# Kernel tuning notes

Hardware: AMD Instinct MI355X
Metric: run time of the kernel (lower is better)

## Reference

```python
import jax, jax.numpy as jnp
import numpy as np

B, L, D, H, Dh = 4, 2048, 1024, 16, 64
DECAY_LR, A_LR, V_LR, G_LR = 64, 64, 32, 128
EPS_GN = 0.00064


def _lora(x, A, Bm, b, act):
    h = x @ A.T
    if act is not None:
        h = act(h)
    y = h @ Bm.T
    return y if b is None else y + b


def setup_inputs() -> dict:
    key = jax.random.key(0)
    ks = jax.random.split(key, 32)
    n = lambda k, shape, s=0.02: (jax.random.normal(k, shape, jnp.float32) * s)
    return {
        "x": n(ks[0], (B, L, D), 1.0),
        "v_first": n(ks[1], (B, L, H, Dh), 1.0),
        "x_r": n(ks[2], (1, 1, D)), "x_w": n(ks[3], (1, 1, D)),
        "x_k": n(ks[4], (1, 1, D)), "x_v": n(ks[5], (1, 1, D)),
        "x_a": n(ks[6], (1, 1, D)), "x_g": n(ks[7], (1, 1, D)),
        "k_k": n(ks[8], (H, Dh), 0.5), "k_a": n(ks[9], (H, Dh), 0.5),
        "r_k": n(ks[10], (H, Dh), 0.5),
        "Wr": n(ks[11], (D, D)), "Wk": n(ks[12], (D, D)),
        "Wv": n(ks[13], (D, D)), "Wo": n(ks[14], (D, D)),
        "gn_w": 1.0 + n(ks[15], (H, Dh)), "gn_b": n(ks[16], (H, Dh)),
        "w_A": n(ks[17], (DECAY_LR, D)), "w_B": n(ks[18], (D, DECAY_LR)), "w_b": n(ks[19], (D,)),
        "v_A": n(ks[20], (V_LR, D)), "v_B": n(ks[21], (D, V_LR)), "v_b": n(ks[22], (D,)),
        "a_A": n(ks[23], (A_LR, D)), "a_B": n(ks[24], (D, A_LR)), "a_b": n(ks[25], (D,)),
        "g_A": n(ks[26], (G_LR, D)), "g_B": n(ks[27], (D, G_LR)),
    }


def reference(x, v_first, x_r, x_w, x_k, x_v, x_a, x_g, k_k, k_a, r_k,
              Wr, Wk, Wv, Wo, gn_w, gn_b,
              w_A, w_B, w_b, v_A, v_B, v_b, a_A, a_B, a_b, g_A, g_B):
    Bx, Lx, Dx = x.shape
    # token shift (no cache -> zero-padded shift)
    x_prev = jnp.concatenate([jnp.zeros_like(x[:, :1]), x[:, :-1]], axis=1)
    xx = x_prev - x
    xr = x + xx * x_r
    xw = x + xx * x_w
    xk = x + xx * x_k
    xv = x + xx * x_v
    xa = x + xx * x_a
    xg = x + xx * x_g

    r = (xr @ Wr.T).reshape(Bx, Lx, H, Dh)
    k = (xk @ Wk.T).reshape(Bx, Lx, H, Dh)
    v = (xv @ Wv.T).reshape(Bx, Lx, H, Dh)
    iclr = jax.nn.sigmoid(_lora(xa, a_A, a_B, a_b, None)).reshape(Bx, Lx, H, Dh)
    gate = _lora(xg, g_A, g_B, None, jax.nn.sigmoid)  # (B,L,D)

    # layer_idx > 0: residual value mixing with v_first
    vv = jax.nn.sigmoid(_lora(xv, v_A, v_B, v_b, None)).reshape(Bx, Lx, H, Dh)
    v = v + (v_first - v) * vv

    w = jnp.exp(-0.606531 * jax.nn.sigmoid(
        _lora(xw, w_A, w_B, w_b, jnp.tanh)).reshape(Bx, Lx, H, Dh))

    kkn = k * k_k
    kk = kkn / jnp.maximum(jnp.linalg.norm(kkn, axis=-1, keepdims=True), 1e-7)
    k = k * (1.0 + (iclr - 1.0) * k_a)
    a = -kk
    b = kk * iclr

    # WKV7 generalized delta-rule scan over time
    def step(state, inp):
        rt, wt, kt, vt, at, bt = inp  # each (B,H,Dh)
        sa = jnp.einsum('bhij,bhj->bhi', state, at)
        state = (state * wt[:, :, None, :]
                 + vt[..., :, None] * kt[..., None, :]
                 + sa[..., :, None] * bt[..., None, :])
        y = jnp.einsum('bhij,bhj->bhi', state, rt)
        return state, y

    tr = lambda z: jnp.swapaxes(z, 0, 1)  # (B,L,H,Dh) -> (L,B,H,Dh)
    state0 = jnp.zeros((Bx, H, Dh, Dh), x.dtype)
    _, ys = jax.lax.scan(step, state0, (tr(r), tr(w), tr(k), tr(v), tr(a), tr(b)))
    out = jnp.swapaxes(ys, 0, 1)  # (B,L,H,Dh)

    # per-head layernorm (group norm), eps = 0.00064
    mean = out.mean(axis=-1, keepdims=True)
    var = out.var(axis=-1, keepdims=True)
    out = gn_w * (out - mean) / jnp.sqrt(var + EPS_GN) + gn_b

    out = out + jnp.sum(r * k * r_k, axis=-1, keepdims=True) * v
    out = out.reshape(Bx, Lx, Dx)
    return (out * gate) @ Wo.T
```

## Files before the change

kernel.cpp:

```cpp
#include <hip/hip_runtime.h>
#include <cmath>


#define DEV __device__ __forceinline__

typedef unsigned short u16;
typedef unsigned int u32;
typedef __bf16 bf16x8 __attribute__((ext_vector_type(8)));
typedef float f32x4 __attribute__((ext_vector_type(4)));

constexpr int Bx = 4, Lx = 2048, Dx = 1024, Hx = 16, Dh = 64;
constexpr int NTOK = Bx * Lx;
constexpr float EPS_GN = 0.00064f;
constexpr int STEP_U16 = 384;
constexpr int TB = 16;
constexpr int NB = Lx / TB;
constexpr int BATCH_U16 = TB * STEP_U16;

DEV float bf2f(u16 u) { union { u32 i; float f; } c; c.i = ((u32)u) << 16; return c.f; }
DEV u16 f2bf(float f) {
    union { float f; u32 i; } c; c.f = f;
    u32 r = c.i + 0x7FFFu + ((c.i >> 16) & 1u);
    return (u16)(r >> 16);
}
DEV void unpack2(u32 u, float& a, float& b) {
    union { u32 i; float f; } c0, c1;
    c0.i = u << 16; c1.i = u & 0xFFFF0000u;
    a = c0.f; b = c1.f;
}

template <int CTRL>
DEV float dpp_add(float v) {
    int p = __builtin_amdgcn_update_dpp(0, __float_as_int(v), CTRL, 0xF, 0xF, true);
    return v + __int_as_float(p);
}

DEV float xor32_add(float x) {
    float a = x, b = x;
    asm volatile("s_nop 1\n\tv_permlane32_swap_b32 %0, %1" : "+v"(a), "+v"(b));
    return a + b;
}

DEV float red32(float x) {
    x = dpp_add<0xB1>(x);
    x = dpp_add<0x4E>(x);
    x = dpp_add<0x141>(x);
    x = dpp_add<0x140>(x);
    return xor32_add(x);
}

__global__ __launch_bounds__(256) void conv_kernel(
    const float* s0, const float* s1, const float* s2, const float* s3,
    const float* s4, const float* s5, const float* s6, const float* s7,
    const float* s8, const float* s9, const float* s10, const float* s11,
    u16* d0, u16* d1, u16* d2, u16* d3, u16* d4, u16* d5, u16* d6, u16* d7,
    u16* d8, u16* d9, u16* d10, u16* d11)
{
    const float* srcs[12] = {s0,s1,s2,s3,s4,s5,s6,s7,s8,s9,s10,s11};
    u16* dsts[12] = {d0,d1,d2,d3,d4,d5,d6,d7,d8,d9,d10,d11};
    const int ns[12] = {65536,65536,32768,32768,65536,65536,131072,131072,
                        1048576,1048576,1048576,1048576};
    int t = blockIdx.y;
    int i = (blockIdx.x * 256 + threadIdx.x) * 4;
    if (i >= ns[t]) return;
    float4 v = *(const float4*)(srcs[t] + i);
    ushort4 o;
    o.x = f2bf(v.x); o.y = f2bf(v.y); o.z = f2bf(v.z); o.w = f2bf(v.w);
    *(ushort4*)(dsts[t] + i) = o;
}

__global__ __launch_bounds__(256) void mix_kernel(
    const float* __restrict__ x,
    const float* __restrict__ mr, const float* __restrict__ mw, const float* __restrict__ mk,
    const float* __restrict__ mv, const float* __restrict__ ma, const float* __restrict__ mg,
    u16* __restrict__ XR, u16* __restrict__ XW, u16* __restrict__ XK,
    u16* __restrict__ XV, u16* __restrict__ XA, u16* __restrict__ XG)
{
    int gi = blockIdx.x * 256 + threadIdx.x;
    int n  = gi >> 8;
    int d4 = (gi & 255) << 2;
    int l  = n & (Lx - 1);
    size_t o = (size_t)n * Dx + d4;
    float4 xc = *(const float4*)(x + o);
    float4 xp = make_float4(0.f, 0.f, 0.f, 0.f);
    if (l != 0) xp = *(const float4*)(x + o - Dx);
    float dx0 = xp.x - xc.x, dx1 = xp.y - xc.y, dx2 = xp.z - xc.z, dx3 = xp.w - xc.w;
    const float* mvs[6] = {mr, mw, mk, mv, ma, mg};
    u16* dsts[6] = {XR, XW, XK, XV, XA, XG};
#pragma unroll
    for (int j = 0; j < 6; ++j) {
        float4 m = *(const float4*)(mvs[j] + d4);
        ushort4 r;
        r.x = f2bf(fmaf(dx0, m.x, xc.x));
        r.y = f2bf(fmaf(dx1, m.y, xc.y));
        r.z = f2bf(fmaf(dx2, m.z, xc.z));
        r.w = f2bf(fmaf(dx3, m.w, xc.w));
        *(ushort4*)(dsts[j] + o) = r;
    }
}

template <int BN, int ACT, bool BIAS, bool F32OUT>
DEV void gemm_body(const u16* __restrict__ A, const u16* __restrict__ B16,
                   const float* __restrict__ bias, void* __restrict__ Cv,
                   int M, int N, int K, int bx, int by)
{
    constexpr int BM = 128, BK = 32;
    constexpr int WGM = (BN == 128) ? 2 : 4;
    constexpr int WGN = (BN == 128) ? 2 : 1;
    constexpr int WTM = BM / WGM, WTN = BN / WGN;
    constexpr int ITM = WTM / 16, ITN = WTN / 16;
    __shared__ __align__(16) u16 Asm[BM * BK];
    __shared__ __align__(16) u16 Bsm[BN * BK];
    const int tid = threadIdx.x;
    const int wid = tid >> 6, lane = tid & 63;
    const int q = lane >> 4, r16 = lane & 15;
    const size_t m0 = (size_t)bx * BM;
    const size_t n0 = (size_t)by * BN;
    const int wm = (wid % WGM) * WTM;
    const int wn = (wid / WGM) * WTN;
    f32x4 acc[ITM][ITN];
    const f32x4 zf = {0.f, 0.f, 0.f, 0.f};
#pragma unroll
    for (int i = 0; i < ITM; ++i)
#pragma unroll
        for (int j = 0; j < ITN; ++j) acc[i][j] = zf;

    for (int k0 = 0; k0 < K; k0 += BK) {
#pragma unroll
        for (int it = 0; it < 2; ++it) {
            int base = it * 2048 + wid * 512;
            int pp = base + lane * 8;
            int row = pp >> 5, col = pp & 31;
            __builtin_amdgcn_global_load_lds(
                (const __attribute__((address_space(1))) void*)(A + (m0 + row) * K + k0 + col),
                (__attribute__((address_space(3))) void*)(Asm + base), 16, 0, 0);
        }
#pragma unroll
        for (int it = 0; it < (BN * BK + 2047) / 2048; ++it) {
            int base = it * 2048 + wid * 512;
            if (BN * BK >= 2048 || base < BN * BK) {
                int pp = base + lane * 8;
                int row = pp >> 5, col = pp & 31;
                __builtin_amdgcn_global_load_lds(
                    (const __attribute__((address_space(1))) void*)(B16 + (n0 + row) * K + k0 + col),
                    (__attribute__((address_space(3))) void*)(Bsm + base), 16, 0, 0);
            }
        }
        __syncthreads();
        bf16x8 af[ITM], bfr[ITN];
#pragma unroll
        for (int im = 0; im < ITM; ++im)
            af[im] = *(const bf16x8*)&Asm[(wm + im * 16 + r16) * BK + q * 8];
#pragma unroll
        for (int in = 0; in < ITN; ++in)
            bfr[in] = *(const bf16x8*)&Bsm[(wn + in * 16 + r16) * BK + q * 8];
#pragma unroll
        for (int im = 0; im < ITM; ++im)
#pragma unroll
            for (int in = 0; in < ITN; ++in)
                acc[im][in] = __builtin_amdgcn_mfma_f32_16x16x32_bf16(af[im], bfr[in], acc[im][in], 0, 0, 0);
        __syncthreads();
    }
#pragma unroll
    for (int im = 0; im < ITM; ++im) {
#pragma unroll
        for (int in = 0; in < ITN; ++in) {
#pragma unroll
            for (int e = 0; e < 4; ++e) {
                size_t row = m0 + wm + im * 16 + q * 4 + e;
                size_t col = n0 + wn + in * 16 + r16;
                float val = acc[im][in][e];
                if constexpr (BIAS) val += bias[col];
                if constexpr (ACT == 1) val = 1.f / (1.f + __expf(-val));
                else if constexpr (ACT == 2) val = tanhf(val);
                else if constexpr (ACT == 3) val = __expf(-0.606531f / (1.f + __expf(-val)));
                if constexpr (F32OUT) ((float*)Cv)[row * (size_t)N + col] = val;
                else ((u16*)Cv)[row * (size_t)N + col] = f2bf(val);
            }
        }
    }
}

template <int BN, int ACT, bool BIAS, bool F32OUT>
__global__ __launch_bounds__(256) void gemm_nt(
    const u16* __restrict__ A, const u16* __restrict__ B16,
    const float* __restrict__ bias, void* __restrict__ Cv,
    int M, int N, int K)
{
    gemm_body<BN, ACT, BIAS, F32OUT>(A, B16, bias, Cv, M, N, K, blockIdx.x, blockIdx.y);
}

__global__ __launch_bounds__(256) void gemm_rkv_kernel(
    const u16* __restrict__ XR, const u16* __restrict__ XK, const u16* __restrict__ XV,
    const u16* __restrict__ Wr16, const u16* __restrict__ Wk16, const u16* __restrict__ Wv16,
    u16* __restrict__ Rbuf, u16* __restrict__ Kbuf, u16* __restrict__ Vbuf)
{
    const u16* A; const u16* Bm; u16* C;
    if (blockIdx.z == 0)      { A = XR; Bm = Wr16; C = Rbuf; }
    else if (blockIdx.z == 1) { A = XK; Bm = Wk16; C = Kbuf; }
    else                      { A = XV; Bm = Wv16; C = Vbuf; }
    gemm_body<128, 0, false, false>(A, Bm, nullptr, C, NTOK, 1024, 1024, blockIdx.x, blockIdx.y);
}

__global__ __launch_bounds__(256) void lora1_kernel(
    const u16* __restrict__ XW, const u16* __restrict__ XA,
    const u16* __restrict__ XV, const u16* __restrict__ XG,
    const u16* __restrict__ wAB, const u16* __restrict__ aAB,
    const u16* __restrict__ vAB, const u16* __restrict__ gAB,
    u16* __restrict__ HW, u16* __restrict__ HA,
    u16* __restrict__ HV, u16* __restrict__ HG)
{
    constexpr int BM = 128, BN = 64, BK = 32, K = 1024;
    constexpr int ITM = 2, ITN = 4;
    const int cfg = blockIdx.y;
    const u16* A; const u16* Bm; u16* C; int ldC, Nv, act;
    if (cfg == 0)      { A = XW; Bm = wAB;            C = HW;      ldC = 64;  Nv = 64; act = 2; }
    else if (cfg == 1) { A = XA; Bm = aAB;            C = HA;      ldC = 64;  Nv = 64; act = 0; }
    else if (cfg == 2) { A = XV; Bm = vAB;            C = HV;      ldC = 32;  Nv = 32; act = 0; }
    else if (cfg == 3) { A = XG; Bm = gAB;            C = HG;      ldC = 128; Nv = 64; act = 1; }
    else               { A = XG; Bm = gAB + 64 * K;   C = HG + 64; ldC = 128; Nv = 64; act = 1; }

    __shared__ __align__(16) u16 Asm[BM * BK];
    __shared__ __align__(16) u16 Bsm[BN * BK];
    const int tid = threadIdx.x;
    const int wid = tid >> 6, lane = tid & 63;
    const int q = lane >> 4, r16 = lane & 15;
    const size_t m0 = (size_t)blockIdx.x * BM;
    const int wm = wid * 32;
    f32x4 acc[ITM][ITN];
    const f32x4 zf = {0.f, 0.f, 0.f, 0.f};
#pragma unroll
    for (int i = 0; i < ITM; ++i)
#pragma unroll
        for (int j = 0; j < ITN; ++j) acc[i][j] = zf;

    for (int k0 = 0; k0 < K; k0 += BK) {
#pragma unroll
        for (int it = 0; it < 2; ++it) {
            int base = it * 2048 + wid * 512;
            int pp = base + lane * 8;
            int row = pp >> 5, col = pp & 31;
            __builtin_amdgcn_global_load_lds(
                (const __attribute__((address_space(1))) void*)(A + (m0 + row) * K + k0 + col),
                (__attribute__((address_space(3))) void*)(Asm + base), 16, 0, 0);
        }
        {
            int base = wid * 512;
            int pp = base + lane * 8;
            int row = pp >> 5, col = pp & 31;
            __builtin_amdgcn_global_load_lds(
                (const __attribute__((address_space(1))) void*)(Bm + row * K + k0 + col),
                (__attribute__((address_space(3))) void*)(Bsm + base), 16, 0, 0);
        }
        __syncthreads();
        bf16x8 af[ITM], bfr[ITN];
#pragma unroll
        for (int im = 0; im < ITM; ++im)
            af[im] = *(const bf16x8*)&Asm[(wm + im * 16 + r16) * BK + q * 8];
#pragma unroll
        for (int in = 0; in < ITN; ++in)
            bfr[in] = *(const bf16x8*)&Bsm[(in * 16 + r16) * BK + q * 8];
#pragma unroll
        for (int im = 0; im < ITM; ++im)
#pragma unroll
            for (int in = 0; in < ITN; ++in)
                acc[im][in] = __builtin_amdgcn_mfma_f32_16x16x32_bf16(af[im], bfr[in], acc[im][in], 0, 0, 0);
        __syncthreads();
    }
#pragma unroll
    for (int im = 0; im < ITM; ++im) {
#pragma unroll
        for (int in = 0; in < ITN; ++in) {
#pragma unroll
            for (int e = 0; e < 4; ++e) {
                size_t row = m0 + wm + im * 16 + q * 4 + e;
                int col = in * 16 + r16;
                if (col < Nv) {
                    float val = acc[im][in][e];
                    if (act == 1) val = 1.f / (1.f + __expf(-val));
                    else if (act == 2) val = tanhf(val);
                    C[row * (size_t)ldC + col] = f2bf(val);
                }
            }
        }
    }
}

__global__ __launch_bounds__(256) void prep_pack_kernel(
    u16* __restrict__ Kb, u16* __restrict__ Vb,
    const u16* __restrict__ Rb, const u16* __restrict__ Wd16,
    const u16* __restrict__ ICLR, const u16* __restrict__ VVb, const float* __restrict__ vfirst,
    const float* __restrict__ k_k, const float* __restrict__ k_a,
    u16* __restrict__ stream)
{
    int g = blockIdx.x * 4 + (threadIdx.x >> 6);
    int lane = threadIdx.x & 63;
    int h = g & (Hx - 1);
    int n = g >> 4;
    size_t idx = (size_t)g * 64 + lane;
    int hd = h * 64 + lane;
    int l = n & (Lx - 1), b = n >> 11;
    size_t so = ((size_t)((b * 16 + h) * Lx + l)) * STEP_U16;

    float k = bf2f(Kb[idx]);
    float iclr = bf2f(ICLR[idx]);
    float kkn = k * k_k[hd];
    float s = kkn * kkn;
#pragma unroll
    for (int off = 32; off > 0; off >>= 1) s += __shfl_xor(s, off, 64);
    float nrm = fmaxf(sqrtf(s), 1e-7f);
    float kk = kkn / nrm;
    u16 knew = f2bf(k * (1.f + (iclr - 1.f) * k_a[hd]));
    float v = bf2f(Vb[idx]), vv = bf2f(VVb[idx]), vf = vfirst[idx];
    u16 vnew = f2bf(fmaf(vf - v, vv, v));
    Kb[idx] = knew;
    Vb[idx] = vnew;
    stream[so + lane]       = Rb[idx];
    stream[so + 64 + lane]  = knew;
    stream[so + 128 + lane] = f2bf(-kk);
    stream[so + 192 + lane] = f2bf(kk * iclr);
    stream[so + 256 + lane] = vnew;
    stream[so + 320 + lane] = Wd16[idx];
}

__global__ __launch_bounds__(256, 2) void scan_kernel(
    const u16* __restrict__ stream, float* __restrict__ Y)
{
    const int bid = blockIdx.x;
    const int xcd = bid & 7, slot = bid >> 3;
    const int bh = xcd + ((slot & 7) << 3);
    const int part = slot >> 3;
    const int tid = threadIdx.x;
    const int lane = tid & 63;
    const int w = tid >> 6;
    const int c = (lane & 15) | ((lane >> 1) & 16);
    const int rhalf = (lane >> 4) & 1;
    const int lr = w * 2 + rhalf;
    const int row = part * 8 + lr;
    const size_t sbase = (size_t)bh * Lx * STEP_U16;
    const size_t ybase = (size_t)(bh >> 4) * ((size_t)Lx * Dx) + (size_t)(bh & 15) * 64;

    __shared__ __align__(16) u16 sbuf[2 * BATCH_U16];
    __shared__ __align__(16) float yp[TB * 8 * 36];

    float S0 = 0.f, S1 = 0.f;

    {
        const u16* g = stream + sbase;
#pragma unroll
        for (int cc = 0; cc < 3; ++cc) {
            const u16* gp = g + (3 * w + cc) * 512 + lane * 8;
            u16* lp = sbuf + (3 * w + cc) * 512;
            __builtin_amdgcn_global_load_lds(
                (const __attribute__((address_space(1))) void*)gp,
                (__attribute__((address_space(3))) void*)lp, 16, 0, 0);
        }
    }

    for (int bt = 0; bt < NB; ++bt) {
        const int cur = bt & 1;
        __syncthreads();
        if (bt + 1 < NB) {
            const u16* g = stream + sbase + (size_t)(bt + 1) * BATCH_U16;
            u16* lbase = sbuf + (1 - cur) * BATCH_U16;
#pragma unroll
            for (int cc = 0; cc < 3; ++cc) {
                const u16* gp = g + (3 * w + cc) * 512 + lane * 8;
                u16* lp = lbase + (3 * w + cc) * 512;
                __builtin_amdgcn_global_load_lds(
                    (const __attribute__((address_space(1))) void*)gp,
                    (__attribute__((address_space(3))) void*)lp, 16, 0, 0);
            }
        }
        const u16* bp = sbuf + cur * BATCH_U16;
        const u16* cp = bp + c * 2;
        u32 r2 = *(const u32*)(cp);
        u32 k2 = *(const u32*)(cp + 64);
        u32 a2 = *(const u32*)(cp + 128);
        u32 b2 = *(const u32*)(cp + 192);
        u32 w2 = *(const u32*)(cp + 320);
        float v = bf2f(bp[256 + row]);
#pragma unroll
        for (int s = 0; s < TB; ++s) {
            u32 nr = 0, nk = 0, na = 0, nb = 0, nw = 0;
            float nv = 0.f;
            if (s + 1 < TB) {
                const u16* np = cp + (s + 1) * STEP_U16;
                nr = *(const u32*)(np);
                nk = *(const u32*)(np + 64);
                na = *(const u32*)(np + 128);
                nb = *(const u32*)(np + 192);
                nw = *(const u32*)(np + 320);
                nv = bf2f(bp[(s + 1) * STEP_U16 + 256 + row]);
            }
            float rr0, rr1, kk0, kk1, aa0, aa1, bb0, bb1, ww0, ww1;
            unpack2(r2, rr0, rr1);
            unpack2(k2, kk0, kk1);
            unpack2(a2, aa0, aa1);
            unpack2(b2, bb0, bb1);
            unpack2(w2, ww0, ww1);
            float sa = fmaf(S1, aa1, S0 * aa0);
            sa = red32(sa);
            float t0 = fmaf(v, kk0, sa * bb0);
            float t1 = fmaf(v, kk1, sa * bb1);
            S0 = fmaf(S0, ww0, t0);
            S1 = fmaf(S1, ww1, t1);
            float y = fmaf(S1, rr1, S0 * rr0);
            yp[(s * 8 + lr) * 36 + c] = y;
            r2 = nr; k2 = nk; a2 = na; b2 = nb; w2 = nw; v = nv;
        }
        __syncthreads();
        if (tid < TB * 8) {
            const float* rp = &yp[tid * 36];
            f32x4 a4 = *(const f32x4*)(rp);
#pragma unroll
            for (int i = 1; i < 8; ++i) {
                f32x4 t4 = *(const f32x4*)(rp + i * 4);
                a4 += t4;
            }
            float yy = (a4[0] + a4[1]) + (a4[2] + a4[3]);
            int s = tid >> 3, j = tid & 7;
            Y[ybase + (size_t)(bt * TB + s) * Dx + part * 8 + j] = yy;
        }
    }
}

__global__ __launch_bounds__(256) void gnorm_kernel(
    const float* __restrict__ Y, const u16* __restrict__ Rb, const u16* __restrict__ Kb,
    const u16* __restrict__ Vb, const float* __restrict__ r_k,
    const float* __restrict__ gnw, const float* __restrict__ gnb,
    u16* __restrict__ GATE_OG)
{
    int g = blockIdx.x * 4 + (threadIdx.x >> 6);
    int lane = threadIdx.x & 63;
    int h = g & (Hx - 1);
    size_t idx = (size_t)g * 64 + lane;
    int hd = h * 64 + lane;
    float y = Y[idx];
    float r = bf2f(Rb[idx]), k = bf2f(Kb[idx]), v = bf2f(Vb[idx]);
    float rkr = r * k * r_k[hd];
    float s1 = y, s2 = y * y, s3 = rkr;
#pragma unroll
    for (int off = 32; off > 0; off >>= 1) {
        s1 += __shfl_xor(s1, off, 64);
        s2 += __shfl_xor(s2, off, 64);
        s3 += __shfl_xor(s3, off, 64);
    }
    float mean = s1 * (1.f / 64.f);
    float var  = s2 * (1.f / 64.f) - mean * mean;
    float inv = 1.f / sqrtf(var + EPS_GN);
    float o = gnw[hd] * ((y - mean) * inv) + gnb[hd];
    o += s3 * v;
    GATE_OG[idx] = f2bf(o * bf2f(GATE_OG[idx]));
}

extern "C" void kernel_launch(void* const* d_in, const int* in_sizes, int n_in,
                              void* d_out, int out_size, void* d_ws, size_t ws_size,
                              hipStream_t stream_)
{
    const float* x      = (const float*)d_in[0];
    const float* vfirst = (const float*)d_in[1];
    const float* x_r = (const float*)d_in[2];
    const float* x_w = (const float*)d_in[3];
    const float* x_k = (const float*)d_in[4];
    const float* x_v = (const float*)d_in[5];
    const float* x_a = (const float*)d_in[6];
    const float* x_g = (const float*)d_in[7];
    const float* k_k = (const float*)d_in[8];
    const float* k_a = (const float*)d_in[9];
    const float* r_k = (const float*)d_in[10];
    const float* Wr  = (const float*)d_in[11];
    const float* Wk  = (const float*)d_in[12];
    const float* Wv  = (const float*)d_in[13];
    const float* Wo  = (const float*)d_in[14];
    const float* gnw = (const float*)d_in[15];
    const float* gnb = (const float*)d_in[16];
    const float* wA  = (const float*)d_in[17];
    const float* wB  = (const float*)d_in[18];
    const float* wb  = (const float*)d_in[19];
    const float* vA  = (const float*)d_in[20];
    const float* vB  = (const float*)d_in[21];
    const float* vb  = (const float*)d_in[22];
    const float* aA  = (const float*)d_in[23];
    const float* aB  = (const float*)d_in[24];
    const float* ab  = (const float*)d_in[25];
    const float* gA  = (const float*)d_in[26];
    const float* gB  = (const float*)d_in[27];

    char* ws = (char*)d_ws;
    const size_t SLOT = (size_t)NTOK * Dx * 2;
    u16* XR = (u16*)(ws + 0 * SLOT);
    u16* XW = (u16*)(ws + 1 * SLOT);
    u16* XK = (u16*)(ws + 2 * SLOT);
    u16* XV = (u16*)(ws + 3 * SLOT);
    u16* XA = (u16*)(ws + 4 * SLOT);
    u16* XG = (u16*)(ws + 5 * SLOT);
    u16* STREAM = (u16*)(ws + 0 * SLOT);
    u16* Rbuf = (u16*)(ws + 6 * SLOT);
    u16* Kbuf = (u16*)(ws + 7 * SLOT);
    u16* Vbuf = (u16*)(ws + 8 * SLOT);
    u16* HW = (u16*)(ws + 9 * SLOT);
    u16* HA = HW + (size_t)NTOK * 64;
    u16* HV = HA + (size_t)NTOK * 64;
    u16* HG = HV + (size_t)NTOK * 32;
    u16* Wo16 = HG + (size_t)NTOK * 128;
    u16* SW = (u16*)(ws + 9 * SLOT + 8 * 1024 * 1024);
    u16* wAB = SW;
    u16* wBB = wAB + 65536;
    u16* vAB = wBB + 65536;
    u16* vBB = vAB + 32768;
    u16* aAB = vBB + 32768;
    u16* aBB = aAB + 65536;
    u16* gAB = aBB + 65536;
    u16* gBB = gAB + 131072;
    u16* Wr16 = (u16*)(ws + 9 * SLOT + 10 * 1024 * 1024);
    u16* Wk16 = Wr16 + 1048576;
    u16* Wv16 = Wk16 + 1048576;
    u16* Wdec16 = (u16*)(ws + 10 * SLOT);
    u16* ICLR   = (u16*)(ws + 11 * SLOT);
    u16* VVb    = (u16*)(ws + 12 * SLOT);
    float* Yb   = (float*)(ws + 10 * SLOT);
    u16* GATE   = (u16*)(ws + 13 * SLOT);

    dim3 blk(256);
    conv_kernel<<<dim3(1024, 12), blk, 0, stream_>>>(
        wA, wB, vA, vB, aA, aB, gA, gB, Wr, Wk, Wv, Wo,
        wAB, wBB, vAB, vBB, aAB, aBB, gAB, gBB, Wr16, Wk16, Wv16, Wo16);
    mix_kernel<<<(NTOK * Dx / 4) / 256, blk, 0, stream_>>>(x, x_r, x_w, x_k, x_v, x_a, x_g,
                                                           XR, XW, XK, XV, XA, XG);
    gemm_rkv_kernel<<<dim3(64, 8, 3), blk, 0, stream_>>>(XR, XK, XV, Wr16, Wk16, Wv16,
                                                         Rbuf, Kbuf, Vbuf);
    lora1_kernel<<<dim3(64, 5), blk, 0, stream_>>>(XW, XA, XV, XG, wAB, aAB, vAB, gAB,
                                                   HW, HA, HV, HG);
    gemm_nt<128, 3, true,  false><<<dim3(64, 8), blk, 0, stream_>>>(HW, wBB, wb, Wdec16, NTOK, 1024, 64);
    gemm_nt<128, 1, true,  false><<<dim3(64, 8), blk, 0, stream_>>>(HA, aBB, ab, ICLR, NTOK, 1024, 64);
    gemm_nt<128, 1, true,  false><<<dim3(64, 8), blk, 0, stream_>>>(HV, vBB, vb, VVb, NTOK, 1024, 32);
    gemm_nt<128, 0, false, false><<<dim3(64, 8), blk, 0, stream_>>>(HG, gBB, nullptr, GATE, NTOK, 1024, 128);

    prep_pack_kernel<<<(NTOK * Hx) / 4, blk, 0, stream_>>>(Kbuf, Vbuf, Rbuf, Wdec16, ICLR, VVb,
                                                           vfirst, k_k, k_a, STREAM);
    scan_kernel<<<512, blk, 0, stream_>>>(STREAM, Yb);
    gnorm_kernel<<<(NTOK * Hx) / 4, blk, 0, stream_>>>(Yb, Rbuf, Kbuf, Vbuf, r_k, gnw, gnb, GATE);
    gemm_nt<128, 0, false, true><<<dim3(64, 8), blk, 0, stream_>>>(GATE, Wo16, nullptr, d_out, NTOK, 1024, 1024);
}
```

Baseline: 706.2 us.

## Merge projection and LoRA launches into grouped kernels, read k/v from stream

Merges the R/K/V projection GEMMs with the first LoRA stage into one grid launch, and the four LoRA up-projection GEMMs into a second launch with a runtime activation selector. prep_pack no longer writes the updated k and v back, so gnorm reads them from the packed scan stream instead. The aim is fewer launches, better occupancy for the small LoRA GEMMs that now run alongside the large ones, and fewer global writes. The cost is runtime branching in the epilogue, and gnorm now does strided reads from the stream buffer.

```diff
diff --git a/kernel.cpp b/kernel.cpp
--- a/kernel.cpp
+++ b/kernel.cpp
@@ -181,52 +181,21 @@
     }
 }
 
-template <int BN, int ACT, bool BIAS, bool F32OUT>
-__global__ __launch_bounds__(256) void gemm_nt(
-    const u16* __restrict__ A, const u16* __restrict__ B16,
-    const float* __restrict__ bias, void* __restrict__ Cv,
-    int M, int N, int K)
-{
-    gemm_body<BN, ACT, BIAS, F32OUT>(A, B16, bias, Cv, M, N, K, blockIdx.x, blockIdx.y);
-}
-
-__global__ __launch_bounds__(256) void gemm_rkv_kernel(
-    const u16* __restrict__ XR, const u16* __restrict__ XK, const u16* __restrict__ XV,
-    const u16* __restrict__ Wr16, const u16* __restrict__ Wk16, const u16* __restrict__ Wv16,
-    u16* __restrict__ Rbuf, u16* __restrict__ Kbuf, u16* __restrict__ Vbuf)
-{
-    const u16* A; const u16* Bm; u16* C;
-    if (blockIdx.z == 0)      { A = XR; Bm = Wr16; C = Rbuf; }
-    else if (blockIdx.z == 1) { A = XK; Bm = Wk16; C = Kbuf; }
-    else                      { A = XV; Bm = Wv16; C = Vbuf; }
-    gemm_body<128, 0, false, false>(A, Bm, nullptr, C, NTOK, 1024, 1024, blockIdx.x, blockIdx.y);
-}
-
-__global__ __launch_bounds__(256) void lora1_kernel(
-    const u16* __restrict__ XW, const u16* __restrict__ XA,
-    const u16* __restrict__ XV, const u16* __restrict__ XG,
-    const u16* __restrict__ wAB, const u16* __restrict__ aAB,
-    const u16* __restrict__ vAB, const u16* __restrict__ gAB,
-    u16* __restrict__ HW, u16* __restrict__ HA,
-    u16* __restrict__ HV, u16* __restrict__ HG)
-{
-    constexpr int BM = 128, BN = 64, BK = 32, K = 1024;
-    constexpr int ITM = 2, ITN = 4;
-    const int cfg = blockIdx.y;
-    const u16* A; const u16* Bm; u16* C; int ldC, Nv, act;
-    if (cfg == 0)      { A = XW; Bm = wAB;            C = HW;      ldC = 64;  Nv = 64; act = 2; }
-    else if (cfg == 1) { A = XA; Bm = aAB;            C = HA;      ldC = 64;  Nv = 64; act = 0; }
-    else if (cfg == 2) { A = XV; Bm = vAB;            C = HV;      ldC = 32;  Nv = 32; act = 0; }
-    else if (cfg == 3) { A = XG; Bm = gAB;            C = HG;      ldC = 128; Nv = 64; act = 1; }
-    else               { A = XG; Bm = gAB + 64 * K;   C = HG + 64; ldC = 128; Nv = 64; act = 1; }
-
+DEV void gemm_body_rt(const u16* __restrict__ A, const u16* __restrict__ B16,
+                      const float* __restrict__ bias, u16* __restrict__ C,
+                      int N, int K, int act, int bx, int by)
+{
+    constexpr int BM = 128, BN = 128, BK = 32;
+    constexpr int ITM = 4, ITN = 4;
     __shared__ __align__(16) u16 Asm[BM * BK];
     __shared__ __align__(16) u16 Bsm[BN * BK];
     const int tid = threadIdx.x;
     const int wid = tid >> 6, lane = tid & 63;
     const int q = lane >> 4, r16 = lane & 15;
-    const size_t m0 = (size_t)blockIdx.x * BM;
-    const int wm = wid * 32;
+    const size_t m0 = (size_t)bx * BM;
+    const size_t n0 = (size_t)by * BN;
+    const int wm = (wid % 2) * 64;
+    const int wn = (wid / 2) * 64;
     f32x4 acc[ITM][ITN];
     const f32x4 zf = {0.f, 0.f, 0.f, 0.f};
 #pragma unroll
@@ -244,22 +213,105 @@
                 (const __attribute__((address_space(1))) void*)(A + (m0 + row) * K + k0 + col),
                 (__attribute__((address_space(3))) void*)(Asm + base), 16, 0, 0);
         }
+#pragma unroll
+        for (int it = 0; it < 2; ++it) {
+            int base = it * 2048 + wid * 512;
+            int pp = base + lane * 8;
+            int row = pp >> 5, col = pp & 31;
+            __builtin_amdgcn_global_load_lds(
+                (const __attribute__((address_space(1))) void*)(B16 + (n0 + row) * K + k0 + col),
+                (__attribute__((address_space(3))) void*)(Bsm + base), 16, 0, 0);
+        }
+        __syncthreads();
+        bf16x8 af[ITM], bfr[ITN];
+#pragma unroll
+        for (int im = 0; im < ITM; ++im)
+            af[im] = *(const bf16x8*)&Asm[(wm + im * 16 + r16) * BK + q * 8];
+#pragma unroll
+        for (int in = 0; in < ITN; ++in)
+            bfr[in] = *(const bf16x8*)&Bsm[(wn + in * 16 + r16) * BK + q * 8];
+#pragma unroll
+        for (int im = 0; im < ITM; ++im)
+#pragma unroll
+            for (int in = 0; in < ITN; ++in)
+                acc[im][in] = __builtin_amdgcn_mfma_f32_16x16x32_bf16(af[im], bfr[in], acc[im][in], 0, 0, 0);
+        __syncthreads();
+    }
+#pragma unroll
+    for (int im = 0; im < ITM; ++im) {
+#pragma unroll
+        for (int in = 0; in < ITN; ++in) {
+#pragma unroll
+            for (int e = 0; e < 4; ++e) {
+                size_t row = m0 + wm + im * 16 + q * 4 + e;
+                size_t col = n0 + wn + in * 16 + r16;
+                float val = acc[im][in][e];
+                if (bias) val += bias[col];
+                if (act == 1) val = 1.f / (1.f + __expf(-val));
+                else if (act == 3) val = __expf(-0.606531f / (1.f + __expf(-val)));
+                C[row * (size_t)N + col] = f2bf(val);
+            }
+        }
+    }
+}
+
+DEV void lora1_body(int cfg,
+    const u16* __restrict__ XW, const u16* __restrict__ XA,
+    const u16* __restrict__ XV, const u16* __restrict__ XG,
+    const u16* __restrict__ wAB, const u16* __restrict__ aAB,
+    const u16* __restrict__ vAB, const u16* __restrict__ gAB,
+    u16* __restrict__ HW, u16* __restrict__ HA,
+    u16* __restrict__ HV, u16* __restrict__ HG, int bx)
+{
+    constexpr int BM = 128, BK = 32, K = 1024;
+    constexpr int ITM = 2, ITN = 4;
+    const u16* A; const u16* Bm; u16* C; int ldC, Nv, act;
+    if (cfg == 0)      { A = XW; Bm = wAB;            C = HW;      ldC = 64;  Nv = 64; act = 2; }
+    else if (cfg == 1) { A = XA; Bm = aAB;            C = HA;      ldC = 64;  Nv = 64; act = 0; }
+    else if (cfg == 2) { A = XV; Bm = vAB;            C = HV;      ldC = 32;  Nv = 32; act = 0; }
+    else if (cfg == 3) { A = XG; Bm = gAB;            C = HG;      ldC = 128; Nv = 64; act = 1; }
+    else               { A = XG; Bm = gAB + 64 * K;   C = HG + 64; ldC = 128; Nv = 64; act = 1; }
+
+    __shared__ __align__(16) u16 Asm1[BM * BK];
+    __shared__ __align__(16) u16 Bsm1[64 * BK];
+    const int tid = threadIdx.x;
+    const int wid = tid >> 6, lane = tid & 63;
+    const int q = lane >> 4, r16 = lane & 15;
+    const size_t m0 = (size_t)bx * BM;
+    const int wm = wid * 32;
+    f32x4 acc[ITM][ITN];
+    const f32x4 zf = {0.f, 0.f, 0.f, 0.f};
+#pragma unroll
+    for (int i = 0; i < ITM; ++i)
+#pragma unroll
+        for (int j = 0; j < ITN; ++j) acc[i][j] = zf;
+
+    for (int k0 = 0; k0 < K; k0 += BK) {
+#pragma unroll
+        for (int it = 0; it < 2; ++it) {
+            int base = it * 2048 + wid * 512;
+            int pp = base + lane * 8;
+            int row = pp >> 5, col = pp & 31;
+            __builtin_amdgcn_global_load_lds(
+                (const __attribute__((address_space(1))) void*)(A + (m0 + row) * K + k0 + col),
+                (__attribute__((address_space(3))) void*)(Asm1 + base), 16, 0, 0);
+        }
         {
             int base = wid * 512;
             int pp = base + lane * 8;
             int row = pp >> 5, col = pp & 31;
             __builtin_amdgcn_global_load_lds(
                 (const __attribute__((address_space(1))) void*)(Bm + row * K + k0 + col),
-                (__attribute__((address_space(3))) void*)(Bsm + base), 16, 0, 0);
+                (__attribute__((address_space(3))) void*)(Bsm1 + base), 16, 0, 0);
         }
         __syncthreads();
         bf16x8 af[ITM], bfr[ITN];
 #pragma unroll
         for (int im = 0; im < ITM; ++im)
-            af[im] = *(const bf16x8*)&Asm[(wm + im * 16 + r16) * BK + q * 8];
+            af[im] = *(const bf16x8*)&Asm1[(wm + im * 16 + r16) * BK + q * 8];
 #pragma unroll
         for (int in = 0; in < ITN; ++in)
-            bfr[in] = *(const bf16x8*)&Bsm[(in * 16 + r16) * BK + q * 8];
+            bfr[in] = *(const bf16x8*)&Bsm1[(in * 16 + r16) * BK + q * 8];
 #pragma unroll
         for (int im = 0; im < ITM; ++im)
 #pragma unroll
@@ -286,8 +338,57 @@
     }
 }
 
+__global__ __launch_bounds__(256) void proj_kernel(
+    const u16* __restrict__ XR, const u16* __restrict__ XK, const u16* __restrict__ XV,
+    const u16* __restrict__ XW, const u16* __restrict__ XA, const u16* __restrict__ XG,
+    const u16* __restrict__ Wr16, const u16* __restrict__ Wk16, const u16* __restrict__ Wv16,
+    const u16* __restrict__ wAB, const u16* __restrict__ aAB,
+    const u16* __restrict__ vAB, const u16* __restrict__ gAB,
+    u16* __restrict__ Rbuf, u16* __restrict__ Kbuf, u16* __restrict__ Vbuf,
+    u16* __restrict__ HW, u16* __restrict__ HA, u16* __restrict__ HV, u16* __restrict__ HG)
+{
+    const int z = blockIdx.z;
+    if (z < 3) {
+        const u16* A; const u16* Bm; u16* C;
+        if (z == 0)      { A = XR; Bm = Wr16; C = Rbuf; }
+        else if (z == 1) { A = XK; Bm = Wk16; C = Kbuf; }
+        else             { A = XV; Bm = Wv16; C = Vbuf; }
+        gemm_body<128, 0, false, false>(A, Bm, nullptr, C, NTOK, 1024, 1024,
+                                        blockIdx.x, blockIdx.y);
+    } else {
+        if (blockIdx.y >= 5) return;
+        lora1_body(blockIdx.y, XW, XA, XV, XG, wAB, aAB, vAB, gAB, HW, HA, HV, HG,
+                   blockIdx.x);
+    }
+}
+
+__global__ __launch_bounds__(256) void lora2_kernel(
+    const u16* __restrict__ HW, const u16* __restrict__ HA,
+    const u16* __restrict__ HV, const u16* __restrict__ HG,
+    const u16* __restrict__ wBB, const u16* __restrict__ aBB,
+    const u16* __restrict__ vBB, const u16* __restrict__ gBB,
+    const float* __restrict__ wb, const float* __restrict__ ab, const float* __restrict__ vb,
+    u16* __restrict__ Wdec16, u16* __restrict__ ICLR,
+    u16* __restrict__ VVb, u16* __restrict__ GATE)
+{
+    const int z = blockIdx.z;
+    const u16* A; const u16* Bm; const float* bias; u16* C; int K, act;
+    if (z == 0)      { A = HW; Bm = wBB; bias = wb;      C = Wdec16; K = 64;  act = 3; }
+    else if (z == 1) { A = HA; Bm = aBB; bias = ab;      C = ICLR;   K = 64;  act = 1; }
+    else if (z == 2) { A = HV; Bm = vBB; bias = vb;      C = VVb;    K = 32;  act = 1; }
+    else             { A = HG; Bm = gBB; bias = nullptr; C = GATE;   K = 128; act = 0; }
+    gemm_body_rt(A, Bm, bias, C, 1024, K, act, blockIdx.x, blockIdx.y);
+}
+
+__global__ __launch_bounds__(256) void gemm_out_kernel(
+    const u16* __restrict__ A, const u16* __restrict__ B16, float* __restrict__ C)
+{
+    gemm_body<128, 0, false, true>(A, B16, nullptr, C, NTOK, 1024, 1024,
+                                   blockIdx.x, blockIdx.y);
+}
+
 __global__ __launch_bounds__(256) void prep_pack_kernel(
-    u16* __restrict__ Kb, u16* __restrict__ Vb,
+    const u16* __restrict__ Kb, const u16* __restrict__ Vb,
     const u16* __restrict__ Rb, const u16* __restrict__ Wd16,
     const u16* __restrict__ ICLR, const u16* __restrict__ VVb, const float* __restrict__ vfirst,
     const float* __restrict__ k_k, const float* __restrict__ k_a,
@@ -313,8 +414,6 @@
     u16 knew = f2bf(k * (1.f + (iclr - 1.f) * k_a[hd]));
     float v = bf2f(Vb[idx]), vv = bf2f(VVb[idx]), vf = vfirst[idx];
     u16 vnew = f2bf(fmaf(vf - v, vv, v));
-    Kb[idx] = knew;
-    Vb[idx] = vnew;
     stream[so + lane]       = Rb[idx];
     stream[so + 64 + lane]  = knew;
     stream[so + 128 + lane] = f2bf(-kk);
@@ -426,18 +525,23 @@
 }
 
 __global__ __launch_bounds__(256) void gnorm_kernel(
-    const float* __restrict__ Y, const u16* __restrict__ Rb, const u16* __restrict__ Kb,
-    const u16* __restrict__ Vb, const float* __restrict__ r_k,
+    const float* __restrict__ Y, const u16* __restrict__ Rb,
+    const u16* __restrict__ stream, const float* __restrict__ r_k,
     const float* __restrict__ gnw, const float* __restrict__ gnb,
     u16* __restrict__ GATE_OG)
 {
     int g = blockIdx.x * 4 + (threadIdx.x >> 6);
     int lane = threadIdx.x & 63;
     int h = g & (Hx - 1);
+    int n = g >> 4;
     size_t idx = (size_t)g * 64 + lane;
     int hd = h * 64 + lane;
+    int l = n & (Lx - 1), b = n >> 11;
+    size_t so = ((size_t)((b * 16 + h) * Lx + l)) * STEP_U16;
     float y = Y[idx];
-    float r = bf2f(Rb[idx]), k = bf2f(Kb[idx]), v = bf2f(Vb[idx]);
+    float r = bf2f(Rb[idx]);
+    float k = bf2f(stream[so + 64 + lane]);
+    float v = bf2f(stream[so + 256 + lane]);
     float rkr = r * k * r_k[hd];
     float s1 = y, s2 = y * y, s3 = rkr;
 #pragma unroll
@@ -528,18 +632,15 @@
         wAB, wBB, vAB, vBB, aAB, aBB, gAB, gBB, Wr16, Wk16, Wv16, Wo16);
     mix_kernel<<<(NTOK * Dx / 4) / 256, blk, 0, stream_>>>(x, x_r, x_w, x_k, x_v, x_a, x_g,
                                                            XR, XW, XK, XV, XA, XG);
-    gemm_rkv_kernel<<<dim3(64, 8, 3), blk, 0, stream_>>>(XR, XK, XV, Wr16, Wk16, Wv16,
-                                                         Rbuf, Kbuf, Vbuf);
-    lora1_kernel<<<dim3(64, 5), blk, 0, stream_>>>(XW, XA, XV, XG, wAB, aAB, vAB, gAB,
-                                                   HW, HA, HV, HG);
-    gemm_nt<128, 3, true,  false><<<dim3(64, 8), blk, 0, stream_>>>(HW, wBB, wb, Wdec16, NTOK, 1024, 64);
-    gemm_nt<128, 1, true,  false><<<dim3(64, 8), blk, 0, stream_>>>(HA, aBB, ab, ICLR, NTOK, 1024, 64);
-    gemm_nt<128, 1, true,  false><<<dim3(64, 8), blk, 0, stream_>>>(HV, vBB, vb, VVb, NTOK, 1024, 32);
-    gemm_nt<128, 0, false, false><<<dim3(64, 8), blk, 0, stream_>>>(HG, gBB, nullptr, GATE, NTOK, 1024, 128);
+    proj_kernel<<<dim3(64, 8, 4), blk, 0, stream_>>>(
+        XR, XK, XV, XW, XA, XG, Wr16, Wk16, Wv16, wAB, aAB, vAB, gAB,
+        Rbuf, Kbuf, Vbuf, HW, HA, HV, HG);
+    lora2_kernel<<<dim3(64, 8, 4), blk, 0, stream_>>>(
+        HW, HA, HV, HG, wBB, aBB, vBB, gBB, wb, ab, vb, Wdec16, ICLR, VVb, GATE);
 
     prep_pack_kernel<<<(NTOK * Hx) / 4, blk, 0, stream_>>>(Kbuf, Vbuf, Rbuf, Wdec16, ICLR, VVb,
                                                            vfirst, k_k, k_a, STREAM);
     scan_kernel<<<512, blk, 0, stream_>>>(STREAM, Yb);
-    gnorm_kernel<<<(NTOK * Hx) / 4, blk, 0, stream_>>>(Yb, Rbuf, Kbuf, Vbuf, r_k, gnw, gnb, GATE);
-    gemm_nt<128, 0, false, true><<<dim3(64, 8), blk, 0, stream_>>>(GATE, Wo16, nullptr, d_out, NTOK, 1024, 1024);
-}
+    gnorm_kernel<<<(NTOK * Hx) / 4, blk, 0, stream_>>>(Yb, Rbuf, STREAM, r_k, gnw, gnb, GATE);
+    gemm_out_kernel<<<dim3(64, 8), blk, 0, stream_>>>(GATE, Wo16, (float*)d_out);
+}
```

Measured after the change: 700.7 us. Within noise of the previous version (-0.8%).
